# Performance work log

Hardware: AMD Instinct MI355X
Metric: run time of the kernel (lower is better)

## Reference

```python
import jax, jax.numpy as jnp
import numpy as np

B, T, DM, H, DK, DV = 2, 2048, 1024, 16, 64, 64


def setup_inputs() -> dict:
    key = jax.random.key(0)
    k = jax.random.split(key, 7)
    std_k = np.float32(1.0 / np.sqrt(DK))
    std_v = np.float32(1.0 / np.sqrt(DV))
    return {
        "xq": jax.random.normal(k[0], (B, T, DM), jnp.float32),
        "xk": jax.random.normal(k[1], (B, T, DM), jnp.float32),
        "xv": jax.random.normal(k[2], (B, T, DM), jnp.float32),
        "mask": jnp.ones((B, T), jnp.float32),  # padding mask: 1 = keep
        "w_q": jax.random.normal(k[3], (H, DM, DK), jnp.float32) * std_k,
        "w_k": jax.random.normal(k[4], (H, DM, DK), jnp.float32) * std_k,
        "w_v": jax.random.normal(k[5], (H, DM, DV), jnp.float32) * std_v,
        "w_o": jax.random.normal(k[6], (H * DV, DM), jnp.float32) * np.float32(1.0 / np.sqrt(H * DV)),
        "b_o": jnp.zeros((DM,), jnp.float32),
    }


def reference(xq, xk, xv, mask, w_q, w_k, w_v, w_o, b_o):
    d_k = w_q.shape[-1]
    # per-head projections: [B,T,DM] x [H,DM,DK] -> [B,H,T,DK]
    q = jnp.einsum('bsd,hdk->bhsk', xq, w_q)
    kk = jnp.einsum('btd,hdk->bhtk', xk, w_k)
    v = jnp.einsum('btd,hdv->bhtv', xv, w_v)
    # NOTE: source divides by d_k (not sqrt(d_k)) -- kept faithful
    scores = jnp.einsum('bhsk,bhtk->bhst', q, kk) / jnp.float32(d_k)
    # _padding_mask: multiply by mask broadcast over key dim, then any exact
    # zero (masked OR coincidentally zero score) becomes -inf -- kept faithful
    masked = scores * mask[:, None, None, :]
    scores = jnp.where(masked == 0.0, -jnp.inf, masked)
    attn = jax.nn.softmax(scores, axis=-1)
    out = jnp.einsum('bhst,bhtv->bhsv', attn, v)  # [B,H,T,DV]
    b, h, t, dv = out.shape
    concat = out.transpose(0, 2, 1, 3).reshape(b, t, h * dv)
    return concat @ w_o + b_o
```

## Files before the change

kernel.cpp:

```cpp
#include <hip/hip_runtime.h>
#include <hip/hip_bf16.h>


typedef __attribute__((ext_vector_type(8))) short short8;
typedef __attribute__((ext_vector_type(4))) short short4v;
typedef __attribute__((ext_vector_type(4))) float f32x4;
typedef __attribute__((ext_vector_type(4))) int i32x4;

__device__ __forceinline__ short f2bf(float f) {
  union { float f; unsigned u; } v; v.f = f;
  unsigned r = v.u + 0x7FFFu + ((v.u >> 16) & 1u);
  return (short)(r >> 16);
}

#define GLD_LDS(g, l) __builtin_amdgcn_global_load_lds( \
    (const __attribute__((address_space(1))) void*)(g), \
    (__attribute__((address_space(3))) void*)(l), 16, 0, 0)

__global__ __launch_bounds__(256) void prep_w_qkv(
    const float* __restrict__ wq, const float* __restrict__ wk,
    const float* __restrict__ wv, short* __restrict__ Wall)
{
  const int z = blockIdx.y;
  const float* w = z == 0 ? wq : (z == 1 ? wk : wv);
  short* Wt = Wall + (size_t)z * 1048576;
  const int h = blockIdx.x >> 4, d0 = (blockIdx.x & 15) * 64;
  const int tid = threadIdx.x;
  __shared__ float Lt[64][65];
#pragma unroll
  for (int it = 0; it < 4; it++) {
    int e = tid + it * 256;
    int dl = e >> 4, k4 = (e & 15) * 4;
    f32x4 v = *(const f32x4*)(w + ((size_t)(h * 1024 + d0 + dl) * 64) + k4);
#pragma unroll
    for (int j = 0; j < 4; j++) Lt[dl][k4 + j] = v[j];
  }
  __syncthreads();
#pragma unroll
  for (int it = 0; it < 4; it++) {
    int e = tid + it * 256;
    int kl = e >> 4, dq = e & 15;
    short4v s;
#pragma unroll
    for (int j = 0; j < 4; j++) s[j] = f2bf(Lt[dq * 4 + j][kl]);
    *(short4v*)(Wt + (size_t)(h * 64 + kl) * 1024 + d0 + dq * 4) = s;
  }
}

__global__ __launch_bounds__(256) void prep_wo(
    const float* __restrict__ wo, short* __restrict__ Wot)
{
  const int k0 = blockIdx.x * 64, n0 = blockIdx.y * 64;
  const int tid = threadIdx.x;
  __shared__ float Lt[64][65];
#pragma unroll
  for (int it = 0; it < 4; it++) {
    int e = tid + it * 256;
    int kl = e >> 4, n4 = (e & 15) * 4;
    f32x4 v = *(const f32x4*)(wo + (size_t)(k0 + kl) * 1024 + n0 + n4);
#pragma unroll
    for (int j = 0; j < 4; j++) Lt[kl][n4 + j] = v[j];
  }
  __syncthreads();
#pragma unroll
  for (int it = 0; it < 4; it++) {
    int e = tid + it * 256;
    int nl = e >> 4, kq = e & 15;
    short4v s;
#pragma unroll
    for (int j = 0; j < 4; j++) s[j] = f2bf(Lt[kq * 4 + j][nl]);
    *(short4v*)(Wot + (size_t)(n0 + nl) * 1024 + k0 + kq * 4) = s;
  }
}

__global__ __launch_bounds__(256) void prep_x(
    const float* __restrict__ xq, const float* __restrict__ xk,
    const float* __restrict__ xv, short* __restrict__ Xb)
{
  const int z = blockIdx.y;
  const float* x = z == 0 ? xq : (z == 1 ? xk : xv);
  size_t i = ((size_t)blockIdx.x * 256 + threadIdx.x) * 8;
  f32x4 f0 = *(const f32x4*)(x + i);
  f32x4 f1 = *(const f32x4*)(x + i + 4);
  short8 s;
#pragma unroll
  for (int j = 0; j < 4; j++) { s[j] = f2bf(f0[j]); s[4 + j] = f2bf(f1[j]); }
  *(short8*)(Xb + (size_t)z * 4194304 + i) = s;
}

__global__ __launch_bounds__(256) void proj_qkv2(
    const short* __restrict__ Xb, const short* __restrict__ Wall,
    short* __restrict__ Qb, short* __restrict__ Kb, short* __restrict__ Vt2)
{
  const int z = blockIdx.z;
  const short* X  = Xb   + (size_t)z * 4194304;
  const short* Wt = Wall + (size_t)z * 1048576;

  const int t0 = blockIdx.x * 128;
  const int n0 = blockIdx.y * 128;
  const int tid = threadIdx.x, w = tid >> 6, lane = tid & 63;
  const int c = lane & 15, q4 = lane >> 4;
  const int wn = (w & 1) * 64, wt = (w >> 1) * 64;
  const int srow = lane >> 2, scol = (lane & 3) * 8;

  __shared__ __align__(16) short Al[128 * 32];
  __shared__ __align__(16) short Bl[128 * 32];

  f32x4 acc[4][4] = {};

  for (int k0 = 0; k0 < 1024; k0 += 32) {
#pragma unroll
    for (int i = 0; i < 2; i++) {
      int rg = (w * 2 + i) * 16;
      GLD_LDS(Wt + (size_t)(n0 + rg + srow) * 1024 + k0 + scol, Al + rg * 32);
      GLD_LDS(X  + (size_t)(t0 + rg + srow) * 1024 + k0 + scol, Bl + rg * 32);
    }
    __syncthreads();
    short8 a[4], bfr[4];
#pragma unroll
    for (int i = 0; i < 4; i++)
      a[i] = *(const short8*)(Al + (wn + i * 16 + c) * 32 + q4 * 8);
#pragma unroll
    for (int j = 0; j < 4; j++)
      bfr[j] = *(const short8*)(Bl + (wt + j * 16 + c) * 32 + q4 * 8);
#pragma unroll
    for (int i = 0; i < 4; i++)
#pragma unroll
      for (int j = 0; j < 4; j++)
        acc[i][j] = __builtin_amdgcn_mfma_f32_16x16x32_bf16(a[i], bfr[j], acc[i][j], 0, 0, 0);
    __syncthreads();
  }

#pragma unroll
  for (int i = 0; i < 4; i++)
#pragma unroll
    for (int j = 0; j < 4; j++) {
      int n = n0 + wn + i * 16 + q4 * 4;
      int trow = t0 + wt + j * 16 + c;
      int b = trow >> 11, t = trow & 2047;
      int h = n >> 6, cc = n & 63;
      int bh = b * 16 + h;
      f32x4 v = acc[i][j];
      short4v pk;
#pragma unroll
      for (int r = 0; r < 4; r++) pk[r] = f2bf(v[r]);
      if (z == 0) {
        *(short4v*)(Qb + (size_t)(bh * 2048 + t) * 64 + cc) = pk;
      } else if (z == 1) {
        *(short4v*)(Kb + (size_t)(bh * 2048 + t) * 64 + cc) = pk;
      } else {
        int t5 = t & 31;
        int kp = ((t5 >> 2) & 3) * 8 + ((t5 >> 4) & 1) * 4 + (t5 & 3);
#pragma unroll
        for (int r = 0; r < 4; r++)
          Vt2[(size_t)bh * 131072 + (t >> 5) * 2048 + (cc + r) * 32 + kp] = pk[r];
      }
    }
}

__global__ __launch_bounds__(128, 2) void attn4(
    const short* __restrict__ Qb, const short* __restrict__ Kb,
    const short* __restrict__ Vt2, const float* __restrict__ mask,
    short* __restrict__ AO)
{
  const int tblk = blockIdx.x;
  const int bh = blockIdx.y;
  const int b = bh >> 4, h = bh & 15;
  const short* Qh = Qb  + (size_t)bh * 131072;
  const short* Kh = Kb  + (size_t)bh * 131072;
  const short* Vh = Vt2 + (size_t)bh * 131072;

  __shared__ __align__(16) short Kl[2][2048];
  __shared__ __align__(16) short Vl[2][2048];

  const int tid = threadIdx.x, w = tid >> 6, lane = tid & 63;
  const int c = lane & 15, q4 = lane >> 4;
  const int qrow0 = tblk * 64 + w * 32;

  short8 qa[2][2];
#pragma unroll
  for (int u = 0; u < 2; u++)
#pragma unroll
    for (int dc = 0; dc < 2; dc++)
      qa[u][dc] = *(const short8*)(Qh + (size_t)(qrow0 + u * 16 + c) * 64 + dc * 32 + q4 * 8);

  f32x4 acc[2][4] = {};
  float l[2] = {0.f, 0.f};

  const int r3 = lane >> 3, c7 = lane & 7;
  const int r2 = lane >> 2, c3 = lane & 3;
  const int kswz = ((c7 ^ r3) & 7) * 8;
  const int vswz = ((c3 ^ ((r2 >> 1) & 3)) & 3) * 8;
  const short* gK = Kh + (size_t)(w * 16 + r3) * 64 + kswz;
  const short* gV = Vh + (size_t)(w * 32 + r2) * 32 + vswz;

  const float LOG2E_64 = 1.44269504088896f * 0.015625f;

#define STAGE(kt, buf) do { \
    const short* kp = gK + (size_t)(kt) * 64; \
    GLD_LDS(kp,           &Kl[buf][w * 1024]); \
    GLD_LDS(kp + 8 * 64,  &Kl[buf][w * 1024 + 512]); \
    const short* vp = gV + (size_t)((kt) >> 5) * 2048; \
    GLD_LDS(vp,           &Vl[buf][w * 1024]); \
    GLD_LDS(vp + 16 * 32, &Vl[buf][w * 1024 + 512]); \
  } while (0)

  STAGE(0, 0);

  for (int i = 0; i < 64; i++) {
    const int kt = i * 32, buf = i & 1;
    __syncthreads();
    if (i < 63) STAGE(kt + 32, buf ^ 1);

    short8 kf[2][2];
#pragma unroll
    for (int s = 0; s < 2; s++)
#pragma unroll
      for (int dc = 0; dc < 2; dc++)
        kf[s][dc] = *(const short8*)(&Kl[buf][(s * 16 + c) * 64 + (((dc * 4 + q4) ^ (c & 7)) & 7) * 8]);

    f32x4 st[2][2] = {};
#pragma unroll
    for (int u = 0; u < 2; u++)
#pragma unroll
      for (int s = 0; s < 2; s++) {
        st[u][s] = __builtin_amdgcn_mfma_f32_16x16x32_bf16(kf[s][0], qa[u][0], st[u][s], 0, 0, 0);
        st[u][s] = __builtin_amdgcn_mfma_f32_16x16x32_bf16(kf[s][1], qa[u][1], st[u][s], 0, 0, 0);
      }

    short8 va[4];
#pragma unroll
    for (int vs = 0; vs < 4; vs++)
      va[vs] = *(const short8*)(&Vl[buf][(vs * 16 + c) * 32 + ((q4 ^ ((c >> 1) & 3)) & 3) * 8]);

    f32x4 cm[2], cb[2];
#pragma unroll
    for (int s = 0; s < 2; s++) {
      f32x4 mk = *(const f32x4*)(mask + b * 2048 + kt + s * 16 + q4 * 4);
      cm[s] = mk * LOG2E_64;
      cb[s] = (mk - 1.0f) * 240.0f;
    }

#pragma unroll
    for (int u = 0; u < 2; u++) {
      unsigned pkd[2][2];
#pragma unroll
      for (int s = 0; s < 2; s++) {
        float e0 = __builtin_amdgcn_exp2f(st[u][s][0] * cm[s][0] + cb[s][0]);
        float e1 = __builtin_amdgcn_exp2f(st[u][s][1] * cm[s][1] + cb[s][1]);
        float e2 = __builtin_amdgcn_exp2f(st[u][s][2] * cm[s][2] + cb[s][2]);
        float e3 = __builtin_amdgcn_exp2f(st[u][s][3] * cm[s][3] + cb[s][3]);
        l[u] += (e0 + e1) + (e2 + e3);
        union { float f; unsigned u; } a0, a1, a2, a3;
        a0.f = e0; a1.f = e1; a2.f = e2; a3.f = e3;
        pkd[s][0] = __builtin_amdgcn_perm(a1.u + 0x8000u, a0.u + 0x8000u, 0x07060302u);
        pkd[s][1] = __builtin_amdgcn_perm(a3.u + 0x8000u, a2.u + 0x8000u, 0x07060302u);
      }
      union { i32x4 i; short8 s; } pb;
      pb.i[0] = (int)pkd[0][0];
      pb.i[1] = (int)pkd[0][1];
      pb.i[2] = (int)pkd[1][0];
      pb.i[3] = (int)pkd[1][1];
#pragma unroll
      for (int vs = 0; vs < 4; vs++)
        acc[u][vs] = __builtin_amdgcn_mfma_f32_16x16x32_bf16(va[vs], pb.s, acc[u][vs], 0, 0, 0);
    }
  }
#undef STAGE

#pragma unroll
  for (int u = 0; u < 2; u++) {
    float lu = l[u];
    lu += __shfl_xor(lu, 16);
    lu += __shfl_xor(lu, 32);
    float inv = 1.0f / lu;
    size_t row = (size_t)b * 2048 + qrow0 + u * 16 + c;
#pragma unroll
    for (int vs = 0; vs < 4; vs++) {
      f32x4 v = acc[u][vs];
      short4v pk;
#pragma unroll
      for (int r = 0; r < 4; r++) pk[r] = f2bf(v[r] * inv);
      *(short4v*)(AO + row * 1024 + h * 64 + vs * 16 + q4 * 4) = pk;
    }
  }
}

__global__ __launch_bounds__(256) void out_proj2(
    const short* __restrict__ AO, const short* __restrict__ Wot,
    const float* __restrict__ bo, float* __restrict__ out)
{
  const int t0 = blockIdx.x * 128;
  const int n0 = blockIdx.y * 128;
  const int tid = threadIdx.x, w = tid >> 6, lane = tid & 63;
  const int c = lane & 15, q4 = lane >> 4;
  const int wn = (w & 1) * 64, wt = (w >> 1) * 64;
  const int srow = lane >> 2, scol = (lane & 3) * 8;

  __shared__ __align__(16) short Al[128 * 32];
  __shared__ __align__(16) short Bl[128 * 32];

  f32x4 acc[4][4] = {};

  for (int k0 = 0; k0 < 1024; k0 += 32) {
#pragma unroll
    for (int i = 0; i < 2; i++) {
      int rg = (w * 2 + i) * 16;
      GLD_LDS(Wot + (size_t)(n0 + rg + srow) * 1024 + k0 + scol, Al + rg * 32);
      GLD_LDS(AO  + (size_t)(t0 + rg + srow) * 1024 + k0 + scol, Bl + rg * 32);
    }
    __syncthreads();
    short8 a[4], bfr[4];
#pragma unroll
    for (int i = 0; i < 4; i++)
      a[i] = *(const short8*)(Al + (wn + i * 16 + c) * 32 + q4 * 8);
#pragma unroll
    for (int j = 0; j < 4; j++)
      bfr[j] = *(const short8*)(Bl + (wt + j * 16 + c) * 32 + q4 * 8);
#pragma unroll
    for (int i = 0; i < 4; i++)
#pragma unroll
      for (int j = 0; j < 4; j++)
        acc[i][j] = __builtin_amdgcn_mfma_f32_16x16x32_bf16(a[i], bfr[j], acc[i][j], 0, 0, 0);
    __syncthreads();
  }

#pragma unroll
  for (int i = 0; i < 4; i++)
#pragma unroll
    for (int j = 0; j < 4; j++) {
      int n = n0 + wn + i * 16 + q4 * 4;
      int trow = t0 + wt + j * 16 + c;
      f32x4 v = acc[i][j] + *(const f32x4*)(bo + n);
      *(f32x4*)(out + (size_t)trow * 1024 + n) = v;
    }
}

extern "C" void kernel_launch(void* const* d_in, const int* in_sizes, int n_in,
                              void* d_out, int out_size, void* d_ws, size_t ws_size,
                              hipStream_t stream)
{
  (void)in_sizes; (void)n_in; (void)out_size; (void)ws_size;
  const float* xq   = (const float*)d_in[0];
  const float* xk   = (const float*)d_in[1];
  const float* xv   = (const float*)d_in[2];
  const float* mask = (const float*)d_in[3];
  const float* wq   = (const float*)d_in[4];
  const float* wk   = (const float*)d_in[5];
  const float* wv   = (const float*)d_in[6];
  const float* wo   = (const float*)d_in[7];
  const float* bo   = (const float*)d_in[8];
  float* out = (float*)d_out;

  char* ws = (char*)d_ws;
  short* Wall = (short*)(ws + (size_t)0);
  short* Wot  = (short*)(ws + ((size_t)6 << 20));
  short* Xb   = (short*)(ws + ((size_t)8 << 20));
  short* AO   = (short*)(ws + ((size_t)8 << 20));
  short* Qb   = (short*)(ws + ((size_t)32 << 20));
  short* Kb   = (short*)(ws + ((size_t)40 << 20));
  short* Vt2  = (short*)(ws + ((size_t)48 << 20));

  prep_w_qkv<<<dim3(256, 3), 256, 0, stream>>>(wq, wk, wv, Wall);
  prep_wo<<<dim3(16, 16), 256, 0, stream>>>(wo, Wot);
  prep_x<<<dim3(2048, 3), 256, 0, stream>>>(xq, xk, xv, Xb);
  proj_qkv2<<<dim3(32, 8, 3), 256, 0, stream>>>(Xb, Wall, Qb, Kb, Vt2);
  attn4<<<dim3(32, 32), 128, 0, stream>>>(Qb, Kb, Vt2, mask, AO);
  out_proj2<<<dim3(32, 8), 256, 0, stream>>>(AO, Wot, bo, out);
}
```

Before: 251.9 us.

## Fuse prep kernels, pre-tile K for direct register loads, drop LDS in attention

The three prep kernels are merged into one launch with a flattened block index. The K projection now writes K in a tiled layout that matches the MFMA fragment order. The attention kernel drops LDS staging and barriers entirely and loads K/V fragments straight from global memory into registers, using manual two-deep software prefetching. Blocks grow to 4 waves covering 128 query rows, which trades LDS sharing between waves for lower sync overhead and relies on L2/cache hits for the K/V reuse across waves.

```diff
diff --git a/kernel.cpp b/kernel.cpp
--- a/kernel.cpp
+++ b/kernel.cpp
@@ -17,80 +17,76 @@
     (const __attribute__((address_space(1))) void*)(g), \
     (__attribute__((address_space(3))) void*)(l), 16, 0, 0)
 
-__global__ __launch_bounds__(256) void prep_w_qkv(
-    const float* __restrict__ wq, const float* __restrict__ wk,
-    const float* __restrict__ wv, short* __restrict__ Wall)
-{
-  const int z = blockIdx.y;
-  const float* w = z == 0 ? wq : (z == 1 ? wk : wv);
-  short* Wt = Wall + (size_t)z * 1048576;
-  const int h = blockIdx.x >> 4, d0 = (blockIdx.x & 15) * 64;
-  const int tid = threadIdx.x;
+__global__ __launch_bounds__(256) void prep_all(
+    const float* __restrict__ xq, const float* __restrict__ xk,
+    const float* __restrict__ xv, const float* __restrict__ wq,
+    const float* __restrict__ wk, const float* __restrict__ wv,
+    const float* __restrict__ wo,
+    short* __restrict__ Xb, short* __restrict__ Wall, short* __restrict__ Wot)
+{
+  const int bx = blockIdx.x, tid = threadIdx.x;
   __shared__ float Lt[64][65];
-#pragma unroll
-  for (int it = 0; it < 4; it++) {
-    int e = tid + it * 256;
-    int dl = e >> 4, k4 = (e & 15) * 4;
-    f32x4 v = *(const f32x4*)(w + ((size_t)(h * 1024 + d0 + dl) * 64) + k4);
-#pragma unroll
-    for (int j = 0; j < 4; j++) Lt[dl][k4 + j] = v[j];
-  }
-  __syncthreads();
-#pragma unroll
-  for (int it = 0; it < 4; it++) {
-    int e = tid + it * 256;
-    int kl = e >> 4, dq = e & 15;
-    short4v s;
-#pragma unroll
-    for (int j = 0; j < 4; j++) s[j] = f2bf(Lt[dq * 4 + j][kl]);
-    *(short4v*)(Wt + (size_t)(h * 64 + kl) * 1024 + d0 + dq * 4) = s;
-  }
-}
-
-__global__ __launch_bounds__(256) void prep_wo(
-    const float* __restrict__ wo, short* __restrict__ Wot)
-{
-  const int k0 = blockIdx.x * 64, n0 = blockIdx.y * 64;
-  const int tid = threadIdx.x;
-  __shared__ float Lt[64][65];
-#pragma unroll
-  for (int it = 0; it < 4; it++) {
-    int e = tid + it * 256;
-    int kl = e >> 4, n4 = (e & 15) * 4;
-    f32x4 v = *(const f32x4*)(wo + (size_t)(k0 + kl) * 1024 + n0 + n4);
-#pragma unroll
-    for (int j = 0; j < 4; j++) Lt[kl][n4 + j] = v[j];
-  }
-  __syncthreads();
-#pragma unroll
-  for (int it = 0; it < 4; it++) {
-    int e = tid + it * 256;
-    int nl = e >> 4, kq = e & 15;
-    short4v s;
-#pragma unroll
-    for (int j = 0; j < 4; j++) s[j] = f2bf(Lt[kq * 4 + j][nl]);
-    *(short4v*)(Wot + (size_t)(n0 + nl) * 1024 + k0 + kq * 4) = s;
-  }
-}
-
-__global__ __launch_bounds__(256) void prep_x(
-    const float* __restrict__ xq, const float* __restrict__ xk,
-    const float* __restrict__ xv, short* __restrict__ Xb)
-{
-  const int z = blockIdx.y;
-  const float* x = z == 0 ? xq : (z == 1 ? xk : xv);
-  size_t i = ((size_t)blockIdx.x * 256 + threadIdx.x) * 8;
-  f32x4 f0 = *(const f32x4*)(x + i);
-  f32x4 f1 = *(const f32x4*)(x + i + 4);
-  short8 s;
-#pragma unroll
-  for (int j = 0; j < 4; j++) { s[j] = f2bf(f0[j]); s[4 + j] = f2bf(f1[j]); }
-  *(short8*)(Xb + (size_t)z * 4194304 + i) = s;
+  if (bx < 6144) {
+    int z = bx >> 11;
+    const float* x = z == 0 ? xq : (z == 1 ? xk : xv);
+    size_t i = ((size_t)(bx & 2047) * 256 + tid) * 8;
+    f32x4 f0 = *(const f32x4*)(x + i);
+    f32x4 f1 = *(const f32x4*)(x + i + 4);
+    short8 s;
+#pragma unroll
+    for (int j = 0; j < 4; j++) { s[j] = f2bf(f0[j]); s[4 + j] = f2bf(f1[j]); }
+    *(short8*)(Xb + (size_t)z * 4194304 + i) = s;
+  } else if (bx < 6912) {
+    int bz = bx - 6144;
+    int z = bz >> 8, inner = bz & 255;
+    const float* w = z == 0 ? wq : (z == 1 ? wk : wv);
+    short* Wt = Wall + (size_t)z * 1048576;
+    int h = inner >> 4, d0 = (inner & 15) * 64;
+#pragma unroll
+    for (int it = 0; it < 4; it++) {
+      int e = tid + it * 256;
+      int dl = e >> 4, k4 = (e & 15) * 4;
+      f32x4 v = *(const f32x4*)(w + ((size_t)(h * 1024 + d0 + dl) * 64) + k4);
+#pragma unroll
+      for (int j = 0; j < 4; j++) Lt[dl][k4 + j] = v[j];
+    }
+    __syncthreads();
+#pragma unroll
+    for (int it = 0; it < 4; it++) {
+      int e = tid + it * 256;
+      int kl = e >> 4, dq = e & 15;
+      short4v s;
+#pragma unroll
+      for (int j = 0; j < 4; j++) s[j] = f2bf(Lt[dq * 4 + j][kl]);
+      *(short4v*)(Wt + (size_t)(h * 64 + kl) * 1024 + d0 + dq * 4) = s;
+    }
+  } else {
+    int bz = bx - 6912;
+    int k0 = (bz >> 4) * 64, n0 = (bz & 15) * 64;
+#pragma unroll
+    for (int it = 0; it < 4; it++) {
+      int e = tid + it * 256;
+      int kl = e >> 4, n4 = (e & 15) * 4;
+      f32x4 v = *(const f32x4*)(wo + (size_t)(k0 + kl) * 1024 + n0 + n4);
+#pragma unroll
+      for (int j = 0; j < 4; j++) Lt[kl][n4 + j] = v[j];
+    }
+    __syncthreads();
+#pragma unroll
+    for (int it = 0; it < 4; it++) {
+      int e = tid + it * 256;
+      int nl = e >> 4, kq = e & 15;
+      short4v s;
+#pragma unroll
+      for (int j = 0; j < 4; j++) s[j] = f2bf(Lt[kq * 4 + j][nl]);
+      *(short4v*)(Wot + (size_t)(n0 + nl) * 1024 + k0 + kq * 4) = s;
+    }
+  }
 }
 
 __global__ __launch_bounds__(256) void proj_qkv2(
     const short* __restrict__ Xb, const short* __restrict__ Wall,
-    short* __restrict__ Qb, short* __restrict__ Kb, short* __restrict__ Vt2)
+    short* __restrict__ Qb, short* __restrict__ Kt2, short* __restrict__ Vt2)
 {
   const int z = blockIdx.z;
   const short* X  = Xb   + (size_t)z * 4194304;
@@ -147,19 +143,26 @@
       if (z == 0) {
         *(short4v*)(Qb + (size_t)(bh * 2048 + t) * 64 + cc) = pk;
       } else if (z == 1) {
-        *(short4v*)(Kb + (size_t)(bh * 2048 + t) * 64 + cc) = pk;
+        int t5 = t & 31, s_ = t5 >> 4, c_ = t5 & 15;
+        size_t base = (size_t)bh * 131072 + (t >> 5) * 2048;
+#pragma unroll
+        for (int r = 0; r < 4; r++) {
+          int dv = cc + r;
+          Kt2[base + ((s_ * 2 + (dv >> 5)) * 16 + c_) * 32 + ((dv >> 3) & 3) * 8 + (dv & 7)] = pk[r];
+        }
       } else {
         int t5 = t & 31;
         int kp = ((t5 >> 2) & 3) * 8 + ((t5 >> 4) & 1) * 4 + (t5 & 3);
+        size_t base = (size_t)bh * 131072 + (t >> 5) * 2048;
 #pragma unroll
         for (int r = 0; r < 4; r++)
-          Vt2[(size_t)bh * 131072 + (t >> 5) * 2048 + (cc + r) * 32 + kp] = pk[r];
+          Vt2[base + (size_t)(cc + r) * 32 + kp] = pk[r];
       }
     }
 }
 
-__global__ __launch_bounds__(128, 2) void attn4(
-    const short* __restrict__ Qb, const short* __restrict__ Kb,
+__global__ __launch_bounds__(256, 2) void attn5(
+    const short* __restrict__ Qb, const short* __restrict__ Kt2,
     const short* __restrict__ Vt2, const float* __restrict__ mask,
     short* __restrict__ AO)
 {
@@ -167,15 +170,12 @@
   const int bh = blockIdx.y;
   const int b = bh >> 4, h = bh & 15;
   const short* Qh = Qb  + (size_t)bh * 131072;
-  const short* Kh = Kb  + (size_t)bh * 131072;
+  const short* Kh = Kt2 + (size_t)bh * 131072;
   const short* Vh = Vt2 + (size_t)bh * 131072;
-
-  __shared__ __align__(16) short Kl[2][2048];
-  __shared__ __align__(16) short Vl[2][2048];
 
   const int tid = threadIdx.x, w = tid >> 6, lane = tid & 63;
   const int c = lane & 15, q4 = lane >> 4;
-  const int qrow0 = tblk * 64 + w * 32;
+  const int qrow0 = tblk * 128 + w * 32;
 
   short8 qa[2][2];
 #pragma unroll
@@ -186,87 +186,72 @@
 
   f32x4 acc[2][4] = {};
   float l[2] = {0.f, 0.f};
-
-  const int r3 = lane >> 3, c7 = lane & 7;
-  const int r2 = lane >> 2, c3 = lane & 3;
-  const int kswz = ((c7 ^ r3) & 7) * 8;
-  const int vswz = ((c3 ^ ((r2 >> 1) & 3)) & 3) * 8;
-  const short* gK = Kh + (size_t)(w * 16 + r3) * 64 + kswz;
-  const short* gV = Vh + (size_t)(w * 32 + r2) * 32 + vswz;
-
   const float LOG2E_64 = 1.44269504088896f * 0.015625f;
 
-#define STAGE(kt, buf) do { \
-    const short* kp = gK + (size_t)(kt) * 64; \
-    GLD_LDS(kp,           &Kl[buf][w * 1024]); \
-    GLD_LDS(kp + 8 * 64,  &Kl[buf][w * 1024 + 512]); \
-    const short* vp = gV + (size_t)((kt) >> 5) * 2048; \
-    GLD_LDS(vp,           &Vl[buf][w * 1024]); \
-    GLD_LDS(vp + 16 * 32, &Vl[buf][w * 1024 + 512]); \
+  const short* kP = Kh + c * 32 + q4 * 8;
+  const short* vP = Vh + c * 32 + q4 * 8;
+  const float* mP = mask + b * 2048 + q4 * 4;
+
+  short8 kf0[2][2], kf1[2][2], va0[4], va1[4];
+
+#define PREF(KF, VA) do { \
+    KF[0][0] = *(const short8*)(kP);        KF[0][1] = *(const short8*)(kP + 512); \
+    KF[1][0] = *(const short8*)(kP + 1024); KF[1][1] = *(const short8*)(kP + 1536); \
+    VA[0] = *(const short8*)(vP);        VA[1] = *(const short8*)(vP + 512); \
+    VA[2] = *(const short8*)(vP + 1024); VA[3] = *(const short8*)(vP + 1536); \
+    kP += 2048; vP += 2048; \
   } while (0)
 
-  STAGE(0, 0);
-
-  for (int i = 0; i < 64; i++) {
-    const int kt = i * 32, buf = i & 1;
-    __syncthreads();
-    if (i < 63) STAGE(kt + 32, buf ^ 1);
-
-    short8 kf[2][2];
-#pragma unroll
-    for (int s = 0; s < 2; s++)
-#pragma unroll
-      for (int dc = 0; dc < 2; dc++)
-        kf[s][dc] = *(const short8*)(&Kl[buf][(s * 16 + c) * 64 + (((dc * 4 + q4) ^ (c & 7)) & 7) * 8]);
-
-    f32x4 st[2][2] = {};
-#pragma unroll
-    for (int u = 0; u < 2; u++)
-#pragma unroll
-      for (int s = 0; s < 2; s++) {
-        st[u][s] = __builtin_amdgcn_mfma_f32_16x16x32_bf16(kf[s][0], qa[u][0], st[u][s], 0, 0, 0);
-        st[u][s] = __builtin_amdgcn_mfma_f32_16x16x32_bf16(kf[s][1], qa[u][1], st[u][s], 0, 0, 0);
-      }
-
-    short8 va[4];
-#pragma unroll
-    for (int vs = 0; vs < 4; vs++)
-      va[vs] = *(const short8*)(&Vl[buf][(vs * 16 + c) * 32 + ((q4 ^ ((c >> 1) & 3)) & 3) * 8]);
-
-    f32x4 cm[2], cb[2];
-#pragma unroll
-    for (int s = 0; s < 2; s++) {
-      f32x4 mk = *(const f32x4*)(mask + b * 2048 + kt + s * 16 + q4 * 4);
-      cm[s] = mk * LOG2E_64;
-      cb[s] = (mk - 1.0f) * 240.0f;
-    }
-
-#pragma unroll
-    for (int u = 0; u < 2; u++) {
-      unsigned pkd[2][2];
-#pragma unroll
-      for (int s = 0; s < 2; s++) {
-        float e0 = __builtin_amdgcn_exp2f(st[u][s][0] * cm[s][0] + cb[s][0]);
-        float e1 = __builtin_amdgcn_exp2f(st[u][s][1] * cm[s][1] + cb[s][1]);
-        float e2 = __builtin_amdgcn_exp2f(st[u][s][2] * cm[s][2] + cb[s][2]);
-        float e3 = __builtin_amdgcn_exp2f(st[u][s][3] * cm[s][3] + cb[s][3]);
-        l[u] += (e0 + e1) + (e2 + e3);
-        union { float f; unsigned u; } a0, a1, a2, a3;
-        a0.f = e0; a1.f = e1; a2.f = e2; a3.f = e3;
-        pkd[s][0] = __builtin_amdgcn_perm(a1.u + 0x8000u, a0.u + 0x8000u, 0x07060302u);
-        pkd[s][1] = __builtin_amdgcn_perm(a3.u + 0x8000u, a2.u + 0x8000u, 0x07060302u);
-      }
-      union { i32x4 i; short8 s; } pb;
-      pb.i[0] = (int)pkd[0][0];
-      pb.i[1] = (int)pkd[0][1];
-      pb.i[2] = (int)pkd[1][0];
-      pb.i[3] = (int)pkd[1][1];
-#pragma unroll
-      for (int vs = 0; vs < 4; vs++)
-        acc[u][vs] = __builtin_amdgcn_mfma_f32_16x16x32_bf16(va[vs], pb.s, acc[u][vs], 0, 0, 0);
-    }
-  }
-#undef STAGE
+#define BODY(KF, VA) do { \
+    f32x4 st[2][2] = {}; \
+    _Pragma("unroll") \
+    for (int u = 0; u < 2; u++) \
+      _Pragma("unroll") \
+      for (int s = 0; s < 2; s++) { \
+        st[u][s] = __builtin_amdgcn_mfma_f32_16x16x32_bf16(KF[s][0], qa[u][0], st[u][s], 0, 0, 0); \
+        st[u][s] = __builtin_amdgcn_mfma_f32_16x16x32_bf16(KF[s][1], qa[u][1], st[u][s], 0, 0, 0); \
+      } \
+    f32x4 cm[2], cb[2]; \
+    _Pragma("unroll") \
+    for (int s = 0; s < 2; s++) { \
+      f32x4 mk = *(const f32x4*)(mP + s * 16); \
+      cm[s] = mk * LOG2E_64; \
+      cb[s] = (mk - 1.0f) * 240.0f; \
+    } \
+    mP += 32; \
+    _Pragma("unroll") \
+    for (int u = 0; u < 2; u++) { \
+      unsigned pkd[2][2]; \
+      _Pragma("unroll") \
+      for (int s = 0; s < 2; s++) { \
+        float e0 = __builtin_amdgcn_exp2f(st[u][s][0] * cm[s][0] + cb[s][0]); \
+        float e1 = __builtin_amdgcn_exp2f(st[u][s][1] * cm[s][1] + cb[s][1]); \
+        float e2 = __builtin_amdgcn_exp2f(st[u][s][2] * cm[s][2] + cb[s][2]); \
+        float e3 = __builtin_amdgcn_exp2f(st[u][s][3] * cm[s][3] + cb[s][3]); \
+        l[u] += (e0 + e1) + (e2 + e3); \
+        union { float f; unsigned u; } a0, a1, a2, a3; \
+        a0.f = e0; a1.f = e1; a2.f = e2; a3.f = e3; \
+        pkd[s][0] = __builtin_amdgcn_perm(a1.u + 0x8000u, a0.u + 0x8000u, 0x07060302u); \
+        pkd[s][1] = __builtin_amdgcn_perm(a3.u + 0x8000u, a2.u + 0x8000u, 0x07060302u); \
+      } \
+      union { i32x4 i; short8 s; } pb; \
+      pb.i[0] = (int)pkd[0][0]; pb.i[1] = (int)pkd[0][1]; \
+      pb.i[2] = (int)pkd[1][0]; pb.i[3] = (int)pkd[1][1]; \
+      _Pragma("unroll") \
+      for (int vs = 0; vs < 4; vs++) \
+        acc[u][vs] = __builtin_amdgcn_mfma_f32_16x16x32_bf16(VA[vs], pb.s, acc[u][vs], 0, 0, 0); \
+    } \
+  } while (0)
+
+  PREF(kf0, va0);
+  for (int ii = 0; ii < 32; ii++) {
+    PREF(kf1, va1);
+    BODY(kf0, va0);
+    if (ii < 31) PREF(kf0, va0);
+    BODY(kf1, va1);
+  }
+#undef PREF
+#undef BODY
 
 #pragma unroll
   for (int u = 0; u < 2; u++) {
@@ -358,13 +343,11 @@
   short* Xb   = (short*)(ws + ((size_t)8 << 20));
   short* AO   = (short*)(ws + ((size_t)8 << 20));
   short* Qb   = (short*)(ws + ((size_t)32 << 20));
-  short* Kb   = (short*)(ws + ((size_t)40 << 20));
+  short* Kt2  = (short*)(ws + ((size_t)40 << 20));
   short* Vt2  = (short*)(ws + ((size_t)48 << 20));
 
-  prep_w_qkv<<<dim3(256, 3), 256, 0, stream>>>(wq, wk, wv, Wall);
-  prep_wo<<<dim3(16, 16), 256, 0, stream>>>(wo, Wot);
-  prep_x<<<dim3(2048, 3), 256, 0, stream>>>(xq, xk, xv, Xb);
-  proj_qkv2<<<dim3(32, 8, 3), 256, 0, stream>>>(Xb, Wall, Qb, Kb, Vt2);
-  attn4<<<dim3(32, 32), 128, 0, stream>>>(Qb, Kb, Vt2, mask, AO);
+  prep_all<<<7168, 256, 0, stream>>>(xq, xk, xv, wq, wk, wv, wo, Xb, Wall, Wot);
+  proj_qkv2<<<dim3(32, 8, 3), 256, 0, stream>>>(Xb, Wall, Qb, Kt2, Vt2);
+  attn5<<<dim3(16, 32), 256, 0, stream>>>(Qb, Kt2, Vt2, mask, AO);
   out_proj2<<<dim3(32, 8), 256, 0, stream>>>(AO, Wot, bo, out);
 }
```

Measured after the change: 243.8 us. 3.2% less time.
